# Kernel optimization log

Hardware: AMD Instinct MI355X
Metric: run time of the kernel (lower is better)

## Reference

```python
import jax, jax.numpy as jnp
import numpy as np
import math
from jax import lax

DIM = 128
D_STATE = 16
D_CONV = 4
EXPAND = 2
NSLICES = 16
D_INNER = EXPAND * DIM          # 256
DT_RANK = math.ceil(DIM / 16)   # 8
B_, H_, W_ = 4, 64, 64
L = H_ * W_                     # 4096


def silu(x):
    return x * jax.nn.sigmoid(x)


def causal_conv1d(x, w, b):
    # x: (b, d, l), w: (d, k) depthwise, b: (d,)  -- causal, output length l
    l = x.shape[-1]
    xp = jnp.pad(x, ((0, 0), (0, 0), (D_CONV - 1, 0)))
    y = sum(w[None, :, k, None] * xp[:, :, k:k + l] for k in range(D_CONV))
    return y + b[None, :, None]


def selective_scan(u, delta, A, B, C):
    # u, delta: (b, d, l); A: (d, n); B, C: (b, n, l)
    bsz, d, l = u.shape
    n = A.shape[1]
    u_t = u.transpose(2, 0, 1)      # (l, b, d)
    d_t = delta.transpose(2, 0, 1)  # (l, b, d)
    B_t = B.transpose(2, 0, 1)      # (l, b, n)
    C_t = C.transpose(2, 0, 1)      # (l, b, n)

    def step(h, inp):
        u_, de_, b_, c_ = inp
        dA = jnp.exp(de_[..., None] * A)                    # (b, d, n)
        h = h * dA + (de_ * u_)[..., None] * b_[:, None, :]  # (b, d, n)
        y = jnp.einsum('bdn,bn->bd', h, c_)
        return h, y

    h0 = jnp.zeros((bsz, d, n), u.dtype)
    _, ys = lax.scan(step, h0, (u_t, d_t, B_t, C_t))
    return ys.transpose(1, 2, 0)  # (b, d, l)


def mamba_dir(xz, conv_w, conv_b, x_proj_w, dt_w, dt_b, A_log, Dp):
    # one directional Mamba branch (conv + S6 scan + silu(z) gating), returns (b, d_inner, l)
    x, z = jnp.split(xz, 2, axis=1)
    x = silu(causal_conv1d(x, conv_w, conv_b))
    x_dbl = jnp.einsum('rd,bdl->brl', x_proj_w, x)          # (b, dt_rank+2n, l)
    dt_raw = x_dbl[:, :DT_RANK]
    Bm = x_dbl[:, DT_RANK:DT_RANK + D_STATE]
    Cm = x_dbl[:, DT_RANK + D_STATE:]
    delta = jax.nn.softplus(jnp.einsum('dr,brl->bdl', dt_w, dt_raw) + dt_b[None, :, None])
    A = -jnp.exp(A_log)
    y = selective_scan(x, delta, A, Bm, Cm)
    y = y + Dp[None, :, None] * x
    return y * silu(z)


def setup_inputs() -> dict:
    key = jax.random.key(0)
    ks = iter(jax.random.split(key, 40))

    def rn(shape, scale=0.02):
        return jax.random.normal(next(ks), shape, dtype=jnp.float32) * scale

    inp = {"x_in": jax.random.normal(next(ks), (B_, H_, W_, DIM), dtype=jnp.float32)}
    inp["in_proj_w"] = rn((2 * D_INNER, DIM))
    for suf in ["", "_b", "_s"]:
        inp["conv_w" + suf] = rn((D_INNER, D_CONV), 0.1)
        inp["conv_b" + suf] = rn((D_INNER,), 0.1)
        inp["x_proj_w" + suf] = rn((DT_RANK + 2 * D_STATE, D_INNER))
        inp["dt_proj_w" + suf] = rn((D_INNER, DT_RANK), 0.1)
        inp["dt_proj_b" + suf] = rn((D_INNER,), 0.1)
        inp["A_log" + suf] = jnp.log(jnp.tile(jnp.arange(1, D_STATE + 1, dtype=jnp.float32), (D_INNER, 1)))
        inp["D" + suf] = jnp.ones((D_INNER,), jnp.float32)
    inp["out_proj_w"] = rn((DIM, D_INNER))
    return inp


def reference(x_in, in_proj_w, conv_w, conv_b, x_proj_w, dt_proj_w, dt_proj_b, A_log, D,
              conv_w_b, conv_b_b, x_proj_w_b, dt_proj_w_b, dt_proj_b_b, A_log_b, D_b,
              conv_w_s, conv_b_s, x_proj_w_s, dt_proj_w_s, dt_proj_b_s, A_log_s, D_s,
              out_proj_w):
    b, h, w, c = x_in.shape
    l = h * w
    x = x_in.reshape(b, l, c)
    xz = jnp.einsum('pd,bld->bpl', in_proj_w, x)  # (b, 2*d_inner, l)

    # forward scan
    y_f = mamba_dir(xz, conv_w, conv_b, x_proj_w, dt_proj_w, dt_proj_b, A_log, D)
    # backward scan (flip along length)
    y_b = jnp.flip(mamba_dir(jnp.flip(xz, -1), conv_w_b, conv_b_b, x_proj_w_b,
                             dt_proj_w_b, dt_proj_b_b, A_log_b, D_b), -1)
    # interleaved-slice scan: chunk length into NSLICES pieces, stack, flatten
    m = l // NSLICES
    xz_s = xz.reshape(b, 2 * D_INNER, NSLICES, m).swapaxes(-1, -2).reshape(b, 2 * D_INNER, l)
    y_s = mamba_dir(xz_s, conv_w_s, conv_b_s, x_proj_w_s, dt_proj_w_s, dt_proj_b_s, A_log_s, D_s)
    y_s = y_s.reshape(b, D_INNER, m, NSLICES).swapaxes(-1, -2).reshape(b, D_INNER, l)

    y = y_f + y_b + y_s
    out = jnp.einsum('od,bdl->blo', out_proj_w, y)
    return out.reshape(b, h, w, c)
```

## Files before the change

### kernel.cpp

```cpp
#include <hip/hip_runtime.h>
#include <math.h>

#define LSEQ 4096

#define XZ_OFF   0ULL
#define XZ_SZ    (4ULL * 512 * 4096)
#define U_OFF    (XZ_OFF + XZ_SZ)
#define DIR_SZ   (4ULL * 256 * 4096)
#define DELTA_OFF (U_OFF + 3ULL * DIR_SZ)
#define BC_OFF   (DELTA_OFF + 3ULL * DIR_SZ)
#define BC_SZ    (4ULL * 4096 * 32)
#define WT_OFF   BC_OFF
#define WTIN_OFF DELTA_OFF

__device__ __forceinline__ float sigmoidf_(float x) { return 1.0f / (1.0f + __expf(-x)); }
__device__ __forceinline__ float siluf_(float x)    { return x * sigmoidf_(x); }
__device__ __forceinline__ float softplusf_(float x){ return (x > 20.0f) ? x : log1pf(__expf(x)); }

__device__ __forceinline__ float fast_exp2(float x) {
    float r;
    asm volatile("v_exp_f32 %0, %1\n\ts_nop 0" : "=v"(r) : "v"(x));
    return r;
}

__device__ __forceinline__ int perm_idx(int dir, int j) {
    if (dir == 0) return j;
    if (dir == 1) return 4095 - j;
    return ((j & 15) << 8) | (j >> 4);
}

#define DPP_MOV(x, ctrl) __int_as_float(__builtin_amdgcn_update_dpp(0, __float_as_int(x), (ctrl), 0xF, 0xF, true))

__global__ __launch_bounds__(256) void transpose_in_kernel(const float* __restrict__ w,
                                                           float* __restrict__ wT) {
    int idx = blockIdx.x * 256 + threadIdx.x;
    int p = idx >> 7, c = idx & 127;
    wT[(size_t)c * 512 + p] = w[(size_t)p * 128 + c];
}

__global__ __launch_bounds__(256) void inproj_kernel(const float* __restrict__ x,
                              const float* __restrict__ wT,
                              float* __restrict__ xz) {
    const int b = blockIdx.y;
    const int l0 = blockIdx.x * 16;
    __shared__ float xs[128 * 20];
    for (int idx = threadIdx.x; idx < 16 * 128; idx += 256) {
        int li = idx >> 7, c = idx & 127;
        xs[c * 20 + li] = x[((size_t)(b * 4096 + l0 + li)) * 128 + c];
    }
    __syncthreads();
    const int p0 = (threadIdx.x & 127) * 4;
    const int g8 = (threadIdx.x >> 7) * 8;
    float acc[4][8];
    #pragma unroll
    for (int j = 0; j < 4; ++j)
        #pragma unroll
        for (int k = 0; k < 8; ++k) acc[j][k] = 0.0f;
    for (int c = 0; c < 128; ++c) {
        float4 wv = *(const float4*)(wT + (size_t)c * 512 + p0);
        const float* xp = xs + c * 20 + g8;
        float4 x0 = *(const float4*)(xp);
        float4 x1 = *(const float4*)(xp + 4);
        float xv[8] = {x0.x, x0.y, x0.z, x0.w, x1.x, x1.y, x1.z, x1.w};
        float wj[4] = {wv.x, wv.y, wv.z, wv.w};
        #pragma unroll
        for (int j = 0; j < 4; ++j)
            #pragma unroll
            for (int k = 0; k < 8; ++k) acc[j][k] += wj[j] * xv[k];
    }
    #pragma unroll
    for (int j = 0; j < 4; ++j) {
        float* op = xz + ((size_t)(b * 512 + p0 + j)) * 4096 + l0 + g8;
        float4 s0; s0.x = acc[j][0]; s0.y = acc[j][1]; s0.z = acc[j][2]; s0.w = acc[j][3];
        float4 s1; s1.x = acc[j][4]; s1.y = acc[j][5]; s1.z = acc[j][6]; s1.w = acc[j][7];
        *(float4*)(op) = s0; *(float4*)(op + 4) = s1;
    }
}

__global__ __launch_bounds__(256) void conv2_kernel(const float* __restrict__ ws_xz,
                                 float* __restrict__ ws_u2,
                                 const float* __restrict__ cw2, const float* __restrict__ cb2) {
    const int d = blockIdx.x, b = blockIdx.y;
    const float* xrow = ws_xz + ((size_t)(b * 512 + d)) * 4096;
    float* urow = ws_u2 + ((size_t)(b * 256 + d)) * 4096;
    __shared__ float sh[16 * 260];
    for (int i = threadIdx.x; i < 4096; i += 256)
        sh[(i >> 8) * 260 + (i & 255)] = xrow[i];
    __syncthreads();
    const float w0 = cw2[d * 4 + 0], w1 = cw2[d * 4 + 1], w2 = cw2[d * 4 + 2], w3 = cw2[d * 4 + 3];
    const float bb = cb2[d];
    const int t = threadIdx.x;
    float xwin[19];
    #pragma unroll
    for (int k = 0; k < 19; ++k) {
        int j = 16 * t - 3 + k;
        xwin[k] = (j >= 0) ? sh[(j & 15) * 260 + (j >> 4)] : 0.0f;
    }
    float r[16];
    #pragma unroll
    for (int i = 0; i < 16; ++i)
        r[i] = siluf_(bb + w0 * xwin[i] + w1 * xwin[i + 1] + w2 * xwin[i + 2] + w3 * xwin[i + 3]);
    #pragma unroll
    for (int q = 0; q < 4; ++q) {
        float4 v; v.x = r[q*4]; v.y = r[q*4+1]; v.z = r[q*4+2]; v.w = r[q*4+3];
        *(float4*)(urow + 16 * t + q * 4) = v;
    }
}

__global__ __launch_bounds__(256) void front_kernel(float* __restrict__ ws,
        const float* __restrict__ xw0, const float* __restrict__ xw1, const float* __restrict__ xw2,
        const float* __restrict__ dw0, const float* __restrict__ dw1, const float* __restrict__ dw2,
        const float* __restrict__ db0, const float* __restrict__ db1, const float* __restrict__ db2,
        const float* __restrict__ cw0, const float* __restrict__ cb0,
        const float* __restrict__ cw1, const float* __restrict__ cb1) {
    const int l0 = blockIdx.x * 32, b = blockIdx.y, dir = blockIdx.z;
    const float* xw = (dir == 0) ? xw0 : (dir == 1) ? xw1 : xw2;
    const float* dw = (dir == 0) ? dw0 : (dir == 1) ? dw1 : dw2;
    const float* db = (dir == 0) ? db0 : (dir == 1) ? db1 : db2;
    const float* xzb = ws + XZ_OFF + (size_t)b * 512 * 4096;
    float* ub      = ws + U_OFF + (size_t)dir * DIR_SZ + (size_t)b * 256 * 4096;
    float* deltab  = ws + DELTA_OFF + (size_t)dir * DIR_SZ + (size_t)b * 256 * 4096;
    float* Bf      = ws + BC_OFF + (size_t)dir * BC_SZ;
    float* Cf      = Bf + BC_SZ / 2;

    __shared__ float xt[256 * 41];
    __shared__ float xd[40 * 33];
    float* ut = xt;

    const int d = threadIdx.x;
    float r[32];

    if (dir != 2) {
        const float* cw = (dir == 0) ? cw0 : cw1;
        const float* cb = (dir == 0) ? cb0 : cb1;
        for (int idx = threadIdx.x; idx < 256 * 9; idx += 256) {
            int dd = idx / 9, i4 = idx - dd * 9;
            int jb = l0 - 4 + i4 * 4;
            float v0 = 0.f, v1 = 0.f, v2 = 0.f, v3 = 0.f;
            if (jb >= 0) {
                if (dir == 0) {
                    float4 v = *(const float4*)(xzb + (size_t)dd * 4096 + jb);
                    v0 = v.x; v1 = v.y; v2 = v.z; v3 = v.w;
                } else {
                    float4 v = *(const float4*)(xzb + (size_t)dd * 4096 + (4092 - jb));
                    v0 = v.w; v1 = v.z; v2 = v.y; v3 = v.x;
                }
            }
            float* xr = xt + dd * 41 + i4 * 4;
            xr[0] = v0; xr[1] = v1; xr[2] = v2; xr[3] = v3;
        }
        __syncthreads();
        const float w0 = cw[d * 4 + 0], w1 = cw[d * 4 + 1], w2 = cw[d * 4 + 2], w3 = cw[d * 4 + 3];
        const float bb = cb[d];
        float win[36];
        #pragma unroll
        for (int k = 0; k < 36; ++k) win[k] = xt[d * 41 + k];
        #pragma unroll
        for (int li = 0; li < 32; ++li)
            r[li] = siluf_(bb + w0 * win[li + 1] + w1 * win[li + 2] + w2 * win[li + 3] + w3 * win[li + 4]);
        float* urow = ub + (size_t)d * 4096 + l0;
        #pragma unroll
        for (int q = 0; q < 8; ++q) {
            float4 v; v.x = r[q*4]; v.y = r[q*4+1]; v.z = r[q*4+2]; v.w = r[q*4+3];
            *(float4*)(urow + q * 4) = v;
        }
        __syncthreads();
    } else {
        const float* urow = ub + (size_t)d * 4096 + l0;
        #pragma unroll
        for (int q = 0; q < 8; ++q) {
            float4 v = *(const float4*)(urow + q * 4);
            r[q*4] = v.x; r[q*4+1] = v.y; r[q*4+2] = v.z; r[q*4+3] = v.w;
        }
        __syncthreads();
    }

    #pragma unroll
    for (int li = 0; li < 32; ++li)
        ut[li * 264 + 4 * (((d >> 2) ^ (li & 7))) + (d & 3)] = r[li];
    __syncthreads();

    {
        const int rg = threadIdx.x >> 5;
        const int li = threadIdx.x & 31;
        float acc[5];
        #pragma unroll
        for (int j = 0; j < 5; ++j) acc[j] = 0.0f;
        const float* up = ut + li * 264;
        const int sw = (li & 7);
        #pragma unroll 2
        for (int c4 = 0; c4 < 64; ++c4) {
            float4 uv = *(const float4*)(up + 4 * (c4 ^ sw));
            const int c = 4 * (c4 ^ sw);
            #pragma unroll
            for (int j = 0; j < 5; ++j) {
                float4 wv = *(const float4*)(xw + (size_t)(rg * 5 + j) * 256 + c);
                acc[j] += wv.x * uv.x + wv.y * uv.y + wv.z * uv.z + wv.w * uv.w;
            }
        }
        #pragma unroll
        for (int j = 0; j < 5; ++j) xd[(rg * 5 + j) * 33 + li] = acc[j];
    }
    __syncthreads();

    {
        const int wv = threadIdx.x >> 6;
        const int lane = threadIdx.x & 63;
        const int n = lane >> 2, lq = lane & 3;
        #pragma unroll
        for (int j = 0; j < 2; ++j) {
            int l4 = (l0 >> 2) + j * 4 + wv;
            int li = (j * 4 + wv) * 4 + lq;
            size_t base = (((size_t)b * 1024 + l4) * 16 + n) * 4 + lq;
            Bf[base] = xd[(8 + n) * 33 + li];
            Cf[base] = xd[(24 + n) * 33 + li];
        }
    }
    {
        const int li = threadIdx.x & 31;
        float xr8[8];
        #pragma unroll
        for (int rr = 0; rr < 8; ++rr) xr8[rr] = xd[rr * 33 + li];
        #pragma unroll
        for (int k = 0; k < 32; ++k) {
            int dd = ((threadIdx.x + k * 256) >> 5);
            float4 wa = *(const float4*)(dw + dd * 8);
            float4 wb = *(const float4*)(dw + dd * 8 + 4);
            float acc = db[dd]
                + wa.x * xr8[0] + wa.y * xr8[1] + wa.z * xr8[2] + wa.w * xr8[3]
                + wb.x * xr8[4] + wb.y * xr8[5] + wb.z * xr8[6] + wb.w * xr8[7];
            deltab[(size_t)dd * 4096 + l0 + li] = softplusf_(acc);
        }
    }
}

__global__ __launch_bounds__(512) void scan_kernel(float* __restrict__ ws,
                            const float* __restrict__ Al0, const float* __restrict__ Dp0,
                            const float* __restrict__ Al1, const float* __restrict__ Dp1,
                            const float* __restrict__ Al2, const float* __restrict__ Dp2) {
    const int d = blockIdx.x, b = blockIdx.y, dir = blockIdx.z;
    const float* Al = (dir == 0) ? Al0 : (dir == 1) ? Al1 : Al2;
    const float* Dp = (dir == 0) ? Dp0 : (dir == 1) ? Dp1 : Dp2;
    const int c = threadIdx.x >> 4;
    const int n = threadIdx.x & 15;
    const int qid = n >> 2;
    const float Ane = -1.44269504f * __expf(Al[d * 16 + n]);
    const float Dd = Dp[d];
    const float* urow = ws + U_OFF + (size_t)dir * DIR_SZ + ((size_t)(b * 256 + d)) * 4096;
    float* drow = ws + DELTA_OFF + (size_t)dir * DIR_SZ + ((size_t)(b * 256 + d)) * 4096;

    __shared__ float sdu[32 * 260];
    __shared__ float red[32 * 34];
    float* Psh = red;
    float* Ssh = red + 512;

    {
        const float4* d4 = (const float4*)drow;
        const float4* u4 = (const float4*)urow;
        for (int i = threadIdx.x; i < 1024; i += 512) {
            float4 dv = d4[i], uv = u4[i];
            int l = i * 4;
            float* p = sdu + (l >> 7) * 260 + (l & 127) * 2;
            float4 a, bq;
            a.x = dv.x; a.y = dv.x * uv.x; a.z = dv.y; a.w = dv.y * uv.y;
            bq.x = dv.z; bq.y = dv.z * uv.z; bq.z = dv.w; bq.w = dv.w * uv.w;
            *(float4*)(p) = a; *(float4*)(p + 4) = bq;
        }
    }
    __syncthreads();

    const float4* Bq = (const float4*)(ws + BC_OFF + (size_t)dir * BC_SZ)
                       + ((size_t)b * 1024 + c * 32) * 16 + n;
    const float4* Cq = (const float4*)(ws + BC_OFF + (size_t)dir * BC_SZ + BC_SZ / 2)
                       + ((size_t)b * 1024 + c * 32) * 16 + n;
    const float4* sp = (const float4*)(sdu + c * 260);

    float S = 0.0f, dsum = 0.0f;
    #pragma unroll 8
    for (int k4 = 0; k4 < 32; ++k4) {
        float4 a = sp[k4 * 2], bq = sp[k4 * 2 + 1];
        float4 Bv = Bq[(size_t)k4 * 16];
        dsum += a.x + a.z + bq.x + bq.z;
        S = S * fast_exp2(Ane * a.x) + a.y * Bv.x;
        S = S * fast_exp2(Ane * a.z) + a.w * Bv.y;
        S = S * fast_exp2(Ane * bq.x) + bq.y * Bv.z;
        S = S * fast_exp2(Ane * bq.z) + bq.w * Bv.w;
    }
    Ssh[c * 16 + n] = S;
    Psh[c * 16 + n] = fast_exp2(Ane * dsum);
    __syncthreads();
    float h = 0.0f;
    for (int k = 0; k < c; ++k) h = h * Psh[k * 16 + n] + Ssh[k * 16 + n];
    __syncthreads();

    #define SCAN_STEP(t, dv, du, Bn, Cn) { \
        h = h * fast_exp2(Ane * (dv)) + (du) * (Bn); \
        float yp = h * (Cn); \
        yp += DPP_MOV(yp, 0xB1); \
        yp += DPP_MOV(yp, 0x4E); \
        red[(4 * (t) + qid) * 34 + c] = yp; }

    for (int g = 0; g < 16; ++g) {
        float4 a0 = sp[g * 4 + 0], a1 = sp[g * 4 + 1];
        float4 a2 = sp[g * 4 + 2], a3 = sp[g * 4 + 3];
        float4 Bv0 = Bq[(size_t)(g * 2) * 16], Bv1 = Bq[(size_t)(g * 2 + 1) * 16];
        float4 Cv0 = Cq[(size_t)(g * 2) * 16], Cv1 = Cq[(size_t)(g * 2 + 1) * 16];
        SCAN_STEP(0, a0.x, a0.y, Bv0.x, Cv0.x)
        SCAN_STEP(1, a0.z, a0.w, Bv0.y, Cv0.y)
        SCAN_STEP(2, a1.x, a1.y, Bv0.z, Cv0.z)
        SCAN_STEP(3, a1.z, a1.w, Bv0.w, Cv0.w)
        SCAN_STEP(4, a2.x, a2.y, Bv1.x, Cv1.x)
        SCAN_STEP(5, a2.z, a2.w, Bv1.y, Cv1.y)
        SCAN_STEP(6, a3.x, a3.y, Bv1.z, Cv1.z)
        SCAN_STEP(7, a3.z, a3.w, Bv1.w, Cv1.w)
        const int tt = n & 7;
        float q0 = red[(4 * tt + 0) * 34 + c];
        float q1 = red[(4 * tt + 1) * 34 + c];
        float q2 = red[(4 * tt + 2) * 34 + c];
        float q3 = red[(4 * tt + 3) * 34 + c];
        float y = (q0 + q1) + (q2 + q3);
        if (n < 8) {
            int gl = c * 128 + g * 8 + n;
            drow[perm_idx(dir, gl)] = y + Dd * urow[gl];
        }
    }
    #undef SCAN_STEP
}

__global__ __launch_bounds__(256) void transpose_w_kernel(const float* __restrict__ ow,
                                                          float* __restrict__ wT) {
    int idx = blockIdx.x * 256 + threadIdx.x;
    int d = idx >> 7, o = idx & 127;
    wT[d * 128 + o] = ow[o * 256 + d];
}

__global__ __launch_bounds__(256) void epilogue_kernel(const float* __restrict__ ws,
                                const float* __restrict__ wT,
                                float* __restrict__ out) {
    const int l0 = blockIdx.x * 32, b = blockIdx.y;
    __shared__ float yt[256][36];
    const float* yf = ws + DELTA_OFF;
    const float* yb = ws + DELTA_OFF + DIR_SZ;
    const float* ysd = ws + DELTA_OFF + 2 * DIR_SZ;

    for (int idx = threadIdx.x; idx < 256 * 32; idx += 256) {
        int d = idx >> 5, li = idx & 31;
        int l = l0 + li;
        size_t ro = ((size_t)(b * 256 + d)) * 4096 + l;
        float z  = ws[XZ_OFF + ((size_t)(b * 512 + 256 + d)) * 4096 + l];
        yt[d][li] = (yf[ro] + yb[ro] + ysd[ro]) * siluf_(z);
    }
    __syncthreads();

    const int o0  = (threadIdx.x & 63) * 2;
    const int li0 = (threadIdx.x >> 6) * 8;
    float accA[8], accB[8];
    #pragma unroll
    for (int k = 0; k < 8; ++k) { accA[k] = 0.0f; accB[k] = 0.0f; }
    for (int d = 0; d < 256; ++d) {
        float2 wv = *(const float2*)(wT + d * 128 + o0);
        float4 y0 = *(const float4*)(&yt[d][li0]);
        float4 y1 = *(const float4*)(&yt[d][li0 + 4]);
        accA[0] += wv.x * y0.x; accA[1] += wv.x * y0.y; accA[2] += wv.x * y0.z; accA[3] += wv.x * y0.w;
        accA[4] += wv.x * y1.x; accA[5] += wv.x * y1.y; accA[6] += wv.x * y1.z; accA[7] += wv.x * y1.w;
        accB[0] += wv.y * y0.x; accB[1] += wv.y * y0.y; accB[2] += wv.y * y0.z; accB[3] += wv.y * y0.w;
        accB[4] += wv.y * y1.x; accB[5] += wv.y * y1.y; accB[6] += wv.y * y1.z; accB[7] += wv.y * y1.w;
    }
    #pragma unroll
    for (int k = 0; k < 8; ++k) {
        float2 st; st.x = accA[k]; st.y = accB[k];
        *(float2*)(out + ((size_t)(b * 4096 + l0 + li0 + k)) * 128 + o0) = st;
    }
}

extern "C" void kernel_launch(void* const* d_in, const int* in_sizes, int n_in,
                              void* d_out, int out_size, void* d_ws, size_t ws_size,
                              hipStream_t stream) {
    const float* x_in = (const float*)d_in[0];
    const float* ipw  = (const float*)d_in[1];
    const float* cw[3]  = {(const float*)d_in[2],  (const float*)d_in[9],  (const float*)d_in[16]};
    const float* cb[3]  = {(const float*)d_in[3],  (const float*)d_in[10], (const float*)d_in[17]};
    const float* xpw[3] = {(const float*)d_in[4],  (const float*)d_in[11], (const float*)d_in[18]};
    const float* dtw[3] = {(const float*)d_in[5],  (const float*)d_in[12], (const float*)d_in[19]};
    const float* dtb[3] = {(const float*)d_in[6],  (const float*)d_in[13], (const float*)d_in[20]};
    const float* alog[3]= {(const float*)d_in[7],  (const float*)d_in[14], (const float*)d_in[21]};
    const float* dp[3]  = {(const float*)d_in[8],  (const float*)d_in[15], (const float*)d_in[22]};
    const float* ow   = (const float*)d_in[23];
    float* ws  = (float*)d_ws;
    float* out = (float*)d_out;

    transpose_in_kernel<<<dim3(256), 256, 0, stream>>>(ipw, ws + WTIN_OFF);
    inproj_kernel<<<dim3(256, 4), 256, 0, stream>>>(x_in, ws + WTIN_OFF, ws);
    conv2_kernel<<<dim3(256, 4), 256, 0, stream>>>(ws, ws + U_OFF + 2 * DIR_SZ, cw[2], cb[2]);
    front_kernel<<<dim3(128, 4, 3), 256, 0, stream>>>(ws,
        xpw[0], xpw[1], xpw[2], dtw[0], dtw[1], dtw[2], dtb[0], dtb[1], dtb[2],
        cw[0], cb[0], cw[1], cb[1]);
    scan_kernel<<<dim3(256, 4, 3), 512, 0, stream>>>(ws,
        alog[0], dp[0], alog[1], dp[1], alog[2], dp[2]);
    transpose_w_kernel<<<dim3(128), 256, 0, stream>>>(ow, ws + WT_OFF);
    epilogue_kernel<<<dim3(128, 4), 256, 0, stream>>>(ws, ws + WT_OFF, out);
}
```

Before: 432.3 us.

## Store xz length-major, fold slice conv into front kernel, drop transpose kernels

The in-projection output becomes length-major, (b, l, 512) instead of (b, 512, l). The front kernel can then gather rows for all three scan orders, including the interleaved-slice permutation, and run the causal conv itself, so the separate conv2 kernel and its round trip of u through memory go away. The scan hoists its exp2 evaluations out of the serial recurrence and uses a builtin exp2 when one is available. The epilogue reads the out-projection weight directly, which removes the transpose_w launch, and it uses smaller length tiles. Risks include strided z reads in the epilogue and uncoalesced per-thread weight row reads.

```diff
diff --git a/kernel.cpp b/kernel.cpp
--- a/kernel.cpp
+++ b/kernel.cpp
@@ -4,24 +4,32 @@
 #define LSEQ 4096
 
 #define XZ_OFF   0ULL
-#define XZ_SZ    (4ULL * 512 * 4096)
+#define XZ_SZ    (4ULL * 4096 * 512)
 #define U_OFF    (XZ_OFF + XZ_SZ)
 #define DIR_SZ   (4ULL * 256 * 4096)
 #define DELTA_OFF (U_OFF + 3ULL * DIR_SZ)
 #define BC_OFF   (DELTA_OFF + 3ULL * DIR_SZ)
 #define BC_SZ    (4ULL * 4096 * 32)
-#define WT_OFF   BC_OFF
 #define WTIN_OFF DELTA_OFF
 
 __device__ __forceinline__ float sigmoidf_(float x) { return 1.0f / (1.0f + __expf(-x)); }
 __device__ __forceinline__ float siluf_(float x)    { return x * sigmoidf_(x); }
 __device__ __forceinline__ float softplusf_(float x){ return (x > 20.0f) ? x : log1pf(__expf(x)); }
 
-__device__ __forceinline__ float fast_exp2(float x) {
+__device__ __forceinline__ float fast_exp2_asm(float x) {
     float r;
     asm volatile("v_exp_f32 %0, %1\n\ts_nop 0" : "=v"(r) : "v"(x));
     return r;
 }
+#if defined(__has_builtin)
+#if __has_builtin(__builtin_amdgcn_exp2f)
+#define EXP2(x) __builtin_amdgcn_exp2f(x)
+#else
+#define EXP2(x) fast_exp2_asm(x)
+#endif
+#else
+#define EXP2(x) fast_exp2_asm(x)
+#endif
 
 __device__ __forceinline__ int perm_idx(int dir, int j) {
     if (dir == 0) return j;
@@ -69,41 +77,9 @@
             for (int k = 0; k < 8; ++k) acc[j][k] += wj[j] * xv[k];
     }
     #pragma unroll
-    for (int j = 0; j < 4; ++j) {
-        float* op = xz + ((size_t)(b * 512 + p0 + j)) * 4096 + l0 + g8;
-        float4 s0; s0.x = acc[j][0]; s0.y = acc[j][1]; s0.z = acc[j][2]; s0.w = acc[j][3];
-        float4 s1; s1.x = acc[j][4]; s1.y = acc[j][5]; s1.z = acc[j][6]; s1.w = acc[j][7];
-        *(float4*)(op) = s0; *(float4*)(op + 4) = s1;
-    }
-}
-
-__global__ __launch_bounds__(256) void conv2_kernel(const float* __restrict__ ws_xz,
-                                 float* __restrict__ ws_u2,
-                                 const float* __restrict__ cw2, const float* __restrict__ cb2) {
-    const int d = blockIdx.x, b = blockIdx.y;
-    const float* xrow = ws_xz + ((size_t)(b * 512 + d)) * 4096;
-    float* urow = ws_u2 + ((size_t)(b * 256 + d)) * 4096;
-    __shared__ float sh[16 * 260];
-    for (int i = threadIdx.x; i < 4096; i += 256)
-        sh[(i >> 8) * 260 + (i & 255)] = xrow[i];
-    __syncthreads();
-    const float w0 = cw2[d * 4 + 0], w1 = cw2[d * 4 + 1], w2 = cw2[d * 4 + 2], w3 = cw2[d * 4 + 3];
-    const float bb = cb2[d];
-    const int t = threadIdx.x;
-    float xwin[19];
-    #pragma unroll
-    for (int k = 0; k < 19; ++k) {
-        int j = 16 * t - 3 + k;
-        xwin[k] = (j >= 0) ? sh[(j & 15) * 260 + (j >> 4)] : 0.0f;
-    }
-    float r[16];
-    #pragma unroll
-    for (int i = 0; i < 16; ++i)
-        r[i] = siluf_(bb + w0 * xwin[i] + w1 * xwin[i + 1] + w2 * xwin[i + 2] + w3 * xwin[i + 3]);
-    #pragma unroll
-    for (int q = 0; q < 4; ++q) {
-        float4 v; v.x = r[q*4]; v.y = r[q*4+1]; v.z = r[q*4+2]; v.w = r[q*4+3];
-        *(float4*)(urow + 16 * t + q * 4) = v;
+    for (int k = 0; k < 8; ++k) {
+        float4 s; s.x = acc[0][k]; s.y = acc[1][k]; s.z = acc[2][k]; s.w = acc[3][k];
+        *(float4*)(xz + ((size_t)(b * 4096 + l0 + g8 + k)) * 512 + p0) = s;
     }
 }
 
@@ -112,68 +88,55 @@
         const float* __restrict__ dw0, const float* __restrict__ dw1, const float* __restrict__ dw2,
         const float* __restrict__ db0, const float* __restrict__ db1, const float* __restrict__ db2,
         const float* __restrict__ cw0, const float* __restrict__ cb0,
-        const float* __restrict__ cw1, const float* __restrict__ cb1) {
+        const float* __restrict__ cw1, const float* __restrict__ cb1,
+        const float* __restrict__ cw2, const float* __restrict__ cb2) {
     const int l0 = blockIdx.x * 32, b = blockIdx.y, dir = blockIdx.z;
     const float* xw = (dir == 0) ? xw0 : (dir == 1) ? xw1 : xw2;
     const float* dw = (dir == 0) ? dw0 : (dir == 1) ? dw1 : dw2;
     const float* db = (dir == 0) ? db0 : (dir == 1) ? db1 : db2;
-    const float* xzb = ws + XZ_OFF + (size_t)b * 512 * 4096;
+    const float* cw = (dir == 0) ? cw0 : (dir == 1) ? cw1 : cw2;
+    const float* cb = (dir == 0) ? cb0 : (dir == 1) ? cb1 : cb2;
+    const float* xzb = ws + XZ_OFF + (size_t)b * 4096 * 512;
     float* ub      = ws + U_OFF + (size_t)dir * DIR_SZ + (size_t)b * 256 * 4096;
     float* deltab  = ws + DELTA_OFF + (size_t)dir * DIR_SZ + (size_t)b * 256 * 4096;
     float* Bf      = ws + BC_OFF + (size_t)dir * BC_SZ;
     float* Cf      = Bf + BC_SZ / 2;
 
-    __shared__ float xt[256 * 41];
+    __shared__ float xt[35 * 260];
     __shared__ float xd[40 * 33];
     float* ut = xt;
 
+    for (int idx = threadIdx.x; idx < 35 * 64; idx += 256) {
+        int k = idx >> 6, dq = idx & 63;
+        int j = l0 - 3 + k;
+        float4 v = {0.f, 0.f, 0.f, 0.f};
+        if (j >= 0) {
+            int row = (dir == 0) ? j : (dir == 1) ? (4095 - j) : (((j & 15) << 8) | (j >> 4));
+            v = *(const float4*)(xzb + (size_t)row * 512 + dq * 4);
+        }
+        *(float4*)(xt + k * 260 + dq * 4) = v;
+    }
+    __syncthreads();
+
     const int d = threadIdx.x;
+    const float w0 = cw[d * 4 + 0], w1 = cw[d * 4 + 1], w2 = cw[d * 4 + 2], w3 = cw[d * 4 + 3];
+    const float bb = cb[d];
+    float win[35];
+    #pragma unroll
+    for (int k = 0; k < 35; ++k) win[k] = xt[k * 260 + d];
     float r[32];
-
-    if (dir != 2) {
-        const float* cw = (dir == 0) ? cw0 : cw1;
-        const float* cb = (dir == 0) ? cb0 : cb1;
-        for (int idx = threadIdx.x; idx < 256 * 9; idx += 256) {
-            int dd = idx / 9, i4 = idx - dd * 9;
-            int jb = l0 - 4 + i4 * 4;
-            float v0 = 0.f, v1 = 0.f, v2 = 0.f, v3 = 0.f;
-            if (jb >= 0) {
-                if (dir == 0) {
-                    float4 v = *(const float4*)(xzb + (size_t)dd * 4096 + jb);
-                    v0 = v.x; v1 = v.y; v2 = v.z; v3 = v.w;
-                } else {
-                    float4 v = *(const float4*)(xzb + (size_t)dd * 4096 + (4092 - jb));
-                    v0 = v.w; v1 = v.z; v2 = v.y; v3 = v.x;
-                }
-            }
-            float* xr = xt + dd * 41 + i4 * 4;
-            xr[0] = v0; xr[1] = v1; xr[2] = v2; xr[3] = v3;
-        }
-        __syncthreads();
-        const float w0 = cw[d * 4 + 0], w1 = cw[d * 4 + 1], w2 = cw[d * 4 + 2], w3 = cw[d * 4 + 3];
-        const float bb = cb[d];
-        float win[36];
-        #pragma unroll
-        for (int k = 0; k < 36; ++k) win[k] = xt[d * 41 + k];
-        #pragma unroll
-        for (int li = 0; li < 32; ++li)
-            r[li] = siluf_(bb + w0 * win[li + 1] + w1 * win[li + 2] + w2 * win[li + 3] + w3 * win[li + 4]);
+    #pragma unroll
+    for (int li = 0; li < 32; ++li)
+        r[li] = siluf_(bb + w0 * win[li] + w1 * win[li + 1] + w2 * win[li + 2] + w3 * win[li + 3]);
+    {
         float* urow = ub + (size_t)d * 4096 + l0;
         #pragma unroll
         for (int q = 0; q < 8; ++q) {
             float4 v; v.x = r[q*4]; v.y = r[q*4+1]; v.z = r[q*4+2]; v.w = r[q*4+3];
             *(float4*)(urow + q * 4) = v;
         }
-        __syncthreads();
-    } else {
-        const float* urow = ub + (size_t)d * 4096 + l0;
-        #pragma unroll
-        for (int q = 0; q < 8; ++q) {
-            float4 v = *(const float4*)(urow + q * 4);
-            r[q*4] = v.x; r[q*4+1] = v.y; r[q*4+2] = v.z; r[q*4+3] = v.w;
-        }
-        __syncthreads();
-    }
+    }
+    __syncthreads();
 
     #pragma unroll
     for (int li = 0; li < 32; ++li)
@@ -280,21 +243,23 @@
     for (int k4 = 0; k4 < 32; ++k4) {
         float4 a = sp[k4 * 2], bq = sp[k4 * 2 + 1];
         float4 Bv = Bq[(size_t)k4 * 16];
-        dsum += a.x + a.z + bq.x + bq.z;
-        S = S * fast_exp2(Ane * a.x) + a.y * Bv.x;
-        S = S * fast_exp2(Ane * a.z) + a.w * Bv.y;
-        S = S * fast_exp2(Ane * bq.x) + bq.y * Bv.z;
-        S = S * fast_exp2(Ane * bq.z) + bq.w * Bv.w;
+        float e0 = EXP2(Ane * a.x), e1 = EXP2(Ane * a.z);
+        float e2 = EXP2(Ane * bq.x), e3 = EXP2(Ane * bq.z);
+        dsum += (a.x + a.z) + (bq.x + bq.z);
+        S = S * e0 + a.y * Bv.x;
+        S = S * e1 + a.w * Bv.y;
+        S = S * e2 + bq.y * Bv.z;
+        S = S * e3 + bq.w * Bv.w;
     }
     Ssh[c * 16 + n] = S;
-    Psh[c * 16 + n] = fast_exp2(Ane * dsum);
+    Psh[c * 16 + n] = EXP2(Ane * dsum);
     __syncthreads();
     float h = 0.0f;
     for (int k = 0; k < c; ++k) h = h * Psh[k * 16 + n] + Ssh[k * 16 + n];
     __syncthreads();
 
-    #define SCAN_STEP(t, dv, du, Bn, Cn) { \
-        h = h * fast_exp2(Ane * (dv)) + (du) * (Bn); \
+    #define SCAN_STEP(t, ee, du, Bn, Cn) { \
+        h = h * (ee) + (du) * (Bn); \
         float yp = h * (Cn); \
         yp += DPP_MOV(yp, 0xB1); \
         yp += DPP_MOV(yp, 0x4E); \
@@ -305,14 +270,18 @@
         float4 a2 = sp[g * 4 + 2], a3 = sp[g * 4 + 3];
         float4 Bv0 = Bq[(size_t)(g * 2) * 16], Bv1 = Bq[(size_t)(g * 2 + 1) * 16];
         float4 Cv0 = Cq[(size_t)(g * 2) * 16], Cv1 = Cq[(size_t)(g * 2 + 1) * 16];
-        SCAN_STEP(0, a0.x, a0.y, Bv0.x, Cv0.x)
-        SCAN_STEP(1, a0.z, a0.w, Bv0.y, Cv0.y)
-        SCAN_STEP(2, a1.x, a1.y, Bv0.z, Cv0.z)
-        SCAN_STEP(3, a1.z, a1.w, Bv0.w, Cv0.w)
-        SCAN_STEP(4, a2.x, a2.y, Bv1.x, Cv1.x)
-        SCAN_STEP(5, a2.z, a2.w, Bv1.y, Cv1.y)
-        SCAN_STEP(6, a3.x, a3.y, Bv1.z, Cv1.z)
-        SCAN_STEP(7, a3.z, a3.w, Bv1.w, Cv1.w)
+        float e0 = EXP2(Ane * a0.x), e1 = EXP2(Ane * a0.z);
+        float e2 = EXP2(Ane * a1.x), e3 = EXP2(Ane * a1.z);
+        float e4 = EXP2(Ane * a2.x), e5 = EXP2(Ane * a2.z);
+        float e6 = EXP2(Ane * a3.x), e7 = EXP2(Ane * a3.z);
+        SCAN_STEP(0, e0, a0.y, Bv0.x, Cv0.x)
+        SCAN_STEP(1, e1, a0.w, Bv0.y, Cv0.y)
+        SCAN_STEP(2, e2, a1.y, Bv0.z, Cv0.z)
+        SCAN_STEP(3, e3, a1.w, Bv0.w, Cv0.w)
+        SCAN_STEP(4, e4, a2.y, Bv1.x, Cv1.x)
+        SCAN_STEP(5, e5, a2.w, Bv1.y, Cv1.y)
+        SCAN_STEP(6, e6, a3.y, Bv1.z, Cv1.z)
+        SCAN_STEP(7, e7, a3.w, Bv1.w, Cv1.w)
         const int tt = n & 7;
         float q0 = red[(4 * tt + 0) * 34 + c];
         float q1 = red[(4 * tt + 1) * 34 + c];
@@ -327,50 +296,53 @@
     #undef SCAN_STEP
 }
 
-__global__ __launch_bounds__(256) void transpose_w_kernel(const float* __restrict__ ow,
-                                                          float* __restrict__ wT) {
-    int idx = blockIdx.x * 256 + threadIdx.x;
-    int d = idx >> 7, o = idx & 127;
-    wT[d * 128 + o] = ow[o * 256 + d];
-}
-
 __global__ __launch_bounds__(256) void epilogue_kernel(const float* __restrict__ ws,
-                                const float* __restrict__ wT,
+                                const float* __restrict__ ow,
                                 float* __restrict__ out) {
-    const int l0 = blockIdx.x * 32, b = blockIdx.y;
-    __shared__ float yt[256][36];
+    const int l0 = blockIdx.x * 16, b = blockIdx.y;
+    __shared__ float yt[256 * 20];
     const float* yf = ws + DELTA_OFF;
     const float* yb = ws + DELTA_OFF + DIR_SZ;
     const float* ysd = ws + DELTA_OFF + 2 * DIR_SZ;
-
-    for (int idx = threadIdx.x; idx < 256 * 32; idx += 256) {
-        int d = idx >> 5, li = idx & 31;
-        int l = l0 + li;
-        size_t ro = ((size_t)(b * 256 + d)) * 4096 + l;
-        float z  = ws[XZ_OFF + ((size_t)(b * 512 + 256 + d)) * 4096 + l];
-        yt[d][li] = (yf[ro] + yb[ro] + ysd[ro]) * siluf_(z);
-    }
-    __syncthreads();
-
-    const int o0  = (threadIdx.x & 63) * 2;
-    const int li0 = (threadIdx.x >> 6) * 8;
-    float accA[8], accB[8];
-    #pragma unroll
-    for (int k = 0; k < 8; ++k) { accA[k] = 0.0f; accB[k] = 0.0f; }
+    const float* xzb = ws + XZ_OFF + (size_t)b * 4096 * 512;
+
+    for (int idx = threadIdx.x; idx < 256 * 4; idx += 256) {
+        int d = idx >> 2, q = (idx & 3) * 4;
+        size_t ro = ((size_t)(b * 256 + d)) * 4096 + l0 + q;
+        float4 vf = *(const float4*)(yf + ro);
+        float4 vb = *(const float4*)(yb + ro);
+        float4 vs = *(const float4*)(ysd + ro);
+        float4 s; s.x = vf.x + vb.x + vs.x; s.y = vf.y + vb.y + vs.y;
+        s.z = vf.z + vb.z + vs.z; s.w = vf.w + vb.w + vs.w;
+        *(float4*)(yt + d * 20 + q) = s;
+    }
+    __syncthreads();
+    {
+        const int d = threadIdx.x;
+        #pragma unroll 4
+        for (int li = 0; li < 16; ++li) {
+            float z = xzb[(size_t)(l0 + li) * 512 + 256 + d];
+            yt[d * 20 + li] *= siluf_(z);
+        }
+    }
+    __syncthreads();
+
+    const int o   = threadIdx.x & 127;
+    const int li0 = (threadIdx.x >> 7) * 8;
+    float acc[8];
+    #pragma unroll
+    for (int k = 0; k < 8; ++k) acc[k] = 0.0f;
+    const float* wrow = ow + (size_t)o * 256;
     for (int d = 0; d < 256; ++d) {
-        float2 wv = *(const float2*)(wT + d * 128 + o0);
-        float4 y0 = *(const float4*)(&yt[d][li0]);
-        float4 y1 = *(const float4*)(&yt[d][li0 + 4]);
-        accA[0] += wv.x * y0.x; accA[1] += wv.x * y0.y; accA[2] += wv.x * y0.z; accA[3] += wv.x * y0.w;
-        accA[4] += wv.x * y1.x; accA[5] += wv.x * y1.y; accA[6] += wv.x * y1.z; accA[7] += wv.x * y1.w;
-        accB[0] += wv.y * y0.x; accB[1] += wv.y * y0.y; accB[2] += wv.y * y0.z; accB[3] += wv.y * y0.w;
-        accB[4] += wv.y * y1.x; accB[5] += wv.y * y1.y; accB[6] += wv.y * y1.z; accB[7] += wv.y * y1.w;
-    }
-    #pragma unroll
-    for (int k = 0; k < 8; ++k) {
-        float2 st; st.x = accA[k]; st.y = accB[k];
-        *(float2*)(out + ((size_t)(b * 4096 + l0 + li0 + k)) * 128 + o0) = st;
-    }
+        float w = wrow[d];
+        float4 y0 = *(const float4*)(yt + d * 20 + li0);
+        float4 y1 = *(const float4*)(yt + d * 20 + li0 + 4);
+        acc[0] += w * y0.x; acc[1] += w * y0.y; acc[2] += w * y0.z; acc[3] += w * y0.w;
+        acc[4] += w * y1.x; acc[5] += w * y1.y; acc[6] += w * y1.z; acc[7] += w * y1.w;
+    }
+    #pragma unroll
+    for (int k = 0; k < 8; ++k)
+        out[((size_t)(b * 4096 + l0 + li0 + k)) * 128 + o] = acc[k];
 }
 
 extern "C" void kernel_launch(void* const* d_in, const int* in_sizes, int n_in,
@@ -391,12 +363,10 @@
 
     transpose_in_kernel<<<dim3(256), 256, 0, stream>>>(ipw, ws + WTIN_OFF);
     inproj_kernel<<<dim3(256, 4), 256, 0, stream>>>(x_in, ws + WTIN_OFF, ws);
-    conv2_kernel<<<dim3(256, 4), 256, 0, stream>>>(ws, ws + U_OFF + 2 * DIR_SZ, cw[2], cb[2]);
     front_kernel<<<dim3(128, 4, 3), 256, 0, stream>>>(ws,
         xpw[0], xpw[1], xpw[2], dtw[0], dtw[1], dtw[2], dtb[0], dtb[1], dtb[2],
-        cw[0], cb[0], cw[1], cb[1]);
+        cw[0], cb[0], cw[1], cb[1], cw[2], cb[2]);
     scan_kernel<<<dim3(256, 4, 3), 512, 0, stream>>>(ws,
         alog[0], dp[0], alog[1], dp[1], alog[2], dp[2]);
-    transpose_w_kernel<<<dim3(128), 256, 0, stream>>>(ow, ws + WT_OFF);
-    epilogue_kernel<<<dim3(128, 4), 256, 0, stream>>>(ws, ws + WT_OFF, out);
-}
+    epilogue_kernel<<<dim3(256, 4), 256, 0, stream>>>(ws, ow, out);
+}
```

Measured after the change: 426.8 us. Within noise of the previous version (-1.3%).
